# Performance work log

Measured on AMD Instinct MI355X. Metric: run time of the kernel, lower is better.

## Reference

```python
import jax, jax.numpy as jnp
import numpy as np

B, T, E, H = 8, 2048, 1024, 64

def setup_inputs() -> dict:
    key = jax.random.key(0)
    k1, k2, k3, k4 = jax.random.split(key, 4)
    x = jax.random.normal(k1, (B, T, E), dtype=jnp.float32)
    # Linear(E, H, bias=False) weights stored as [E, H] (x @ W)
    s = 1.0 / np.sqrt(E)
    Wk = jax.random.normal(k2, (E, H), dtype=jnp.float32) * s
    Wq = jax.random.normal(k3, (E, H), dtype=jnp.float32) * s
    Wv = jax.random.normal(k4, (E, H), dtype=jnp.float32) * s
    return {"x": x, "Wk": Wk, "Wq": Wq, "Wv": Wv}

def reference(x, Wk, Wq, Wv):
    _, t, e = x.shape
    k = jnp.einsum('bte,eh->bth', x, Wk)
    q = jnp.einsum('bte,eh->bth', x, Wq)
    v = jnp.einsum('bte,eh->bth', x, Wv)
    # NOTE: original scales by E**-0.5 (embedding dim), not head_size**-0.5
    wei = jnp.einsum('bqh,bkh->bqk', q, k) * (e ** -0.5)
    causal = jnp.tril(jnp.ones((t, t), dtype=bool))
    wei = jnp.where(causal, wei, -jnp.inf)
    wei = jax.nn.softmax(wei, axis=-1)
    out = jnp.einsum('bqk,bkh->bqh', wei, v)
    return out
```

## Files before the change

### kernel.cpp

```cpp
#include <hip/hip_runtime.h>

typedef unsigned short u16;
typedef unsigned int u32;
typedef __bf16 bf16x8 __attribute__((ext_vector_type(8)));
typedef __bf16 bf16x4 __attribute__((ext_vector_type(4)));
typedef float f32x4 __attribute__((ext_vector_type(4)));

constexpr int Bn = 8, Tn = 2048, En = 1024, Hn = 64;
constexpr int Mrows = Bn * Tn;
constexpr float CEXP = 0.03125f * 1.4426950408889634f;

__device__ __forceinline__ u16 f2bf(float f) {
  u32 u = __float_as_uint(f);
  return (u16)((u + 0x7fffu + ((u >> 16) & 1u)) >> 16);
}

__device__ __forceinline__ void gload16(const void* g, void* l) {
  __builtin_amdgcn_global_load_lds(
      (const __attribute__((address_space(1))) void*)g,
      (__attribute__((address_space(3))) void*)l, 16, 0, 0);
}

__global__ __launch_bounds__(256) void wt_kernel(
    const float* __restrict__ Wk, const float* __restrict__ Wq,
    const float* __restrict__ Wv, u16* __restrict__ Wt) {
  __shared__ u16 tile[64][72];
  const int mat = blockIdx.x >> 4;
  const int k0 = (blockIdx.x & 15) * 64;
  const float* W = (mat == 0) ? Wk : (mat == 1) ? Wq : Wv;
  const int t = threadIdx.x;
  {
    const int kl = t >> 2;
    const int h0 = (t & 3) * 16;
    const float4* src = (const float4*)(W + (size_t)(k0 + kl) * Hn + h0);
#pragma unroll
    for (int i = 0; i < 4; ++i) {
      float4 v = src[i];
      tile[h0 + 4 * i + 0][kl] = f2bf(v.x);
      tile[h0 + 4 * i + 1][kl] = f2bf(v.y);
      tile[h0 + 4 * i + 2][kl] = f2bf(v.z);
      tile[h0 + 4 * i + 3][kl] = f2bf(v.w);
    }
  }
  __syncthreads();
  {
    const int hl = t >> 2;
    const int kk = (t & 3) * 16;
    uint4 a = *(const uint4*)&tile[hl][kk];
    uint4 b = *(const uint4*)&tile[hl][kk + 8];
    u16* dst = Wt + (size_t)mat * Hn * En + (size_t)hl * En + k0 + kk;
    *(uint4*)dst = a;
    *(uint4*)(dst + 8) = b;
  }
}

__global__ __launch_bounds__(256, 2) void qkv_kernel(
    const float* __restrict__ x, const u16* __restrict__ Wt,
    u16* __restrict__ Kb16, u16* __restrict__ Qb16, u16* __restrict__ Vt16) {
  constexpr int BK = 64;
  __shared__ __align__(16) float xs[3][32 * BK];
  const int t = threadIdx.x;
  const int w = t >> 6, lane = t & 63;
  const int quad = lane >> 4, l16 = lane & 15;
  const int r0 = blockIdx.x * 32;

  const int rj0 = w * 8 + (lane >> 4);
  const int rj1 = rj0 + 4;
  const float* gsrc0 = x + (size_t)(r0 + rj0) * En + (((lane & 15) ^ (rj0 & 15)) << 2);
  const float* gsrc1 = x + (size_t)(r0 + rj1) * En + (((lane & 15) ^ (rj1 & 15)) << 2);

  const u16* wpb = Wt + (size_t)l16 * En + quad * 8;

  int ofs[2][2];
#pragma unroll
  for (int ks = 0; ks < 2; ++ks) {
    ofs[ks][0] = ((ks * 8 + quad * 2) ^ l16) << 2;
    ofs[ks][1] = ((ks * 8 + quad * 2 + 1) ^ l16) << 2;
  }

  f32x4 acc[3][2];
#pragma unroll
  for (int i = 0; i < 3; ++i)
#pragma unroll
    for (int nt = 0; nt < 2; ++nt) acc[i][nt] = (f32x4){0.f, 0.f, 0.f, 0.f};

  bf16x8 afA[3][2], afB[3][2];

#define STAGE(P, K0)                              \
  do {                                            \
    gload16(gsrc0 + (K0), (P) + w * 512);         \
    gload16(gsrc1 + (K0), (P) + w * 512 + 256);   \
  } while (0)

#define LOADA(DST, K0)                                                              \
  do {                                                                              \
    _Pragma("unroll") for (int i_ = 0; i_ < 3; ++i_)                                \
        _Pragma("unroll") for (int ks_ = 0; ks_ < 2; ++ks_)                         \
            DST[i_][ks_] = *(const bf16x8*)(wpb + (size_t)((3 * w + i_) * 16) * En + \
                                            (K0) + ks_ * 32);                       \
  } while (0)

#define CVT8(LO, HI, R)                                       \
  do {                                                        \
    R[0] = (__bf16)LO[0]; R[1] = (__bf16)LO[1];               \
    R[2] = (__bf16)LO[2]; R[3] = (__bf16)LO[3];               \
    R[4] = (__bf16)HI[0]; R[5] = (__bf16)HI[1];               \
    R[6] = (__bf16)HI[2]; R[7] = (__bf16)HI[3];               \
  } while (0)

#define COMPUTE(P, AF)                                                             \
  do {                                                                             \
    const float* xa_ = (P) + l16 * 64;                                             \
    const float* xb_ = (P) + (l16 + 16) * 64;                                      \
    _Pragma("unroll") for (int ks_ = 0; ks_ < 2; ++ks_) {                          \
      f32x4 lo0_ = *(const f32x4*)(xa_ + ofs[ks_][0]);                             \
      f32x4 hi0_ = *(const f32x4*)(xa_ + ofs[ks_][1]);                             \
      f32x4 lo1_ = *(const f32x4*)(xb_ + ofs[ks_][0]);                             \
      f32x4 hi1_ = *(const f32x4*)(xb_ + ofs[ks_][1]);                             \
      bf16x8 b0_, b1_;                                                             \
      CVT8(lo0_, hi0_, b0_);                                                       \
      CVT8(lo1_, hi1_, b1_);                                                       \
      _Pragma("unroll") for (int i_ = 0; i_ < 3; ++i_) {                           \
        acc[i_][0] = __builtin_amdgcn_mfma_f32_16x16x32_bf16(AF[i_][ks_], b0_,     \
                                                             acc[i_][0], 0, 0, 0); \
        acc[i_][1] = __builtin_amdgcn_mfma_f32_16x16x32_bf16(AF[i_][ks_], b1_,     \
                                                             acc[i_][1], 0, 0, 0); \
      }                                                                            \
    }                                                                              \
  } while (0)

#define WAITBAR(N)                                          \
  do {                                                      \
    asm volatile("s_waitcnt vmcnt(" #N ")" ::: "memory");   \
    __builtin_amdgcn_s_barrier();                           \
    asm volatile("" ::: "memory");                          \
  } while (0)

  float* p0 = &xs[0][0];
  float* p1 = &xs[1][0];
  float* p2 = &xs[2][0];

  STAGE(p0, 0);
  STAGE(p1, BK);
  LOADA(afA, 0);

  for (int tt = 0; tt < 16; tt += 2) {
    WAITBAR(8);
    LOADA(afB, (tt + 1) * 64);
    asm volatile("" ::: "memory");
    if (tt + 2 < 16) STAGE(p2, (tt + 2) * 64);
    COMPUTE(p0, afA);

    if (tt == 14) {
      WAITBAR(6);
    } else {
      WAITBAR(8);
    }
    if (tt + 2 < 16) LOADA(afA, (tt + 2) * 64);
    asm volatile("" ::: "memory");
    if (tt + 3 < 16) STAGE(p0, (tt + 3) * 64);
    COMPUTE(p1, afB);

    float* tmp = p0; p0 = p2; p2 = p1; p1 = tmp;
  }

#undef STAGE
#undef LOADA
#undef CVT8
#undef COMPUTE
#undef WAITBAR

#pragma unroll
  for (int i = 0; i < 3; ++i) {
    const int mt = 3 * w + i;
    const int mat = mt >> 2, ht = mt & 3;
#pragma unroll
    for (int nt = 0; nt < 2; ++nt) {
      const int row = r0 + nt * 16 + l16;
      f32x4 a = acc[i][nt];
      if (mat < 2) {
        u16* dst = ((mat == 0) ? Kb16 : Qb16) + (size_t)row * Hn + ht * 16 + quad * 4;
        uint2 pk;
        pk.x = (u32)f2bf(a[0]) | ((u32)f2bf(a[1]) << 16);
        pk.y = (u32)f2bf(a[2]) | ((u32)f2bf(a[3]) << 16);
        *(uint2*)dst = pk;
      } else {
        const int bb = row >> 11, tt = row & 2047;
        u16* base = Vt16 + ((size_t)bb * 64) * Tn + tt;
#pragma unroll
        for (int r = 0; r < 4; ++r)
          base[(size_t)(ht * 16 + quad * 4 + r) * Tn] = f2bf(a[r]);
      }
    }
  }
}

__global__ __launch_bounds__(256, 2) void attn_kernel(
    const u16* __restrict__ Qb16, const u16* __restrict__ Kb16,
    const u16* __restrict__ Vt16, float* __restrict__ out) {
  __shared__ u16 pt[2][4][2][16][40];
  __shared__ float l_sh[2][4][16];
  __shared__ float o_sh[2][4][16][68];

  const int idx = blockIdx.x;
  const int b = idx & 7;
  const int tq = 63 - (idx >> 3);
  const int w = threadIdx.x >> 6, lane = threadIdx.x & 63;
  const int quad = lane >> 4, l16 = lane & 15;
  const int qbase = tq * 32;
  const int limit = qbase + 32;
  const int ch = ((limit + 127) >> 7) << 5;
  const int lo = w * ch;
  const int hi = min(lo + ch, limit);
  const int qa_abs = qbase + l16;
  const int qb_abs = qbase + 16 + l16;

  const u16* Kp = Kb16 + (size_t)b * Tn * Hn;
  const u16* Vp = Vt16 + (size_t)b * 64 * Tn;

  const u16* qrowA = Qb16 + ((size_t)b * Tn + qa_abs) * Hn + quad * 8;
  const u16* qrowB = qrowA + (size_t)16 * Hn;
  const bf16x8 qa0 = *(const bf16x8*)(qrowA);
  const bf16x8 qa1 = *(const bf16x8*)(qrowA + 32);
  const bf16x8 qb0 = *(const bf16x8*)(qrowB);
  const bf16x8 qb1 = *(const bf16x8*)(qrowB + 32);

  f32x4 oA0 = {0.f, 0.f, 0.f, 0.f}, oA1 = oA0, oA2 = oA0, oA3 = oA0;
  f32x4 oB0 = oA0, oB1 = oA0, oB2 = oA0, oB3 = oA0;
  f32x4 laccA = oA0, laccB = oA0;

#pragma unroll 2
  for (int kb = lo; kb < hi; kb += 32) {
    const int par = (kb >> 5) & 1;
    const u16* krow0 = Kp + (size_t)(kb + l16) * Hn + quad * 8;
    const u16* krow1 = krow0 + (size_t)16 * Hn;
    const bf16x8 k0lo = *(const bf16x8*)(krow0);
    const bf16x8 k0hi = *(const bf16x8*)(krow0 + 32);
    const bf16x8 k1lo = *(const bf16x8*)(krow1);
    const bf16x8 k1hi = *(const bf16x8*)(krow1 + 32);

    const f32x4 z = {0.f, 0.f, 0.f, 0.f};
    f32x4 s0a = __builtin_amdgcn_mfma_f32_16x16x32_bf16(k0lo, qa0, z, 0, 0, 0);
    s0a = __builtin_amdgcn_mfma_f32_16x16x32_bf16(k0hi, qa1, s0a, 0, 0, 0);
    f32x4 s1a = __builtin_amdgcn_mfma_f32_16x16x32_bf16(k1lo, qa0, z, 0, 0, 0);
    s1a = __builtin_amdgcn_mfma_f32_16x16x32_bf16(k1hi, qa1, s1a, 0, 0, 0);
    f32x4 s0b = __builtin_amdgcn_mfma_f32_16x16x32_bf16(k0lo, qb0, z, 0, 0, 0);
    s0b = __builtin_amdgcn_mfma_f32_16x16x32_bf16(k0hi, qb1, s0b, 0, 0, 0);
    f32x4 s1b = __builtin_amdgcn_mfma_f32_16x16x32_bf16(k1lo, qb0, z, 0, 0, 0);
    s1b = __builtin_amdgcn_mfma_f32_16x16x32_bf16(k1hi, qb1, s1b, 0, 0, 0);

    if (kb + 15 > qbase) {
#pragma unroll
      for (int r = 0; r < 4; ++r)
        if (kb + quad * 4 + r > qa_abs) s0a[r] = -3.0e38f;
    }
    if (kb + 31 > qbase) {
#pragma unroll
      for (int r = 0; r < 4; ++r)
        if (kb + 16 + quad * 4 + r > qa_abs) s1a[r] = -3.0e38f;
    }
    if (kb + 15 > qbase + 16) {
#pragma unroll
      for (int r = 0; r < 4; ++r)
        if (kb + quad * 4 + r > qb_abs) s0b[r] = -3.0e38f;
    }
    if (kb + 31 > qbase + 16) {
#pragma unroll
      for (int r = 0; r < 4; ++r)
        if (kb + 16 + quad * 4 + r > qb_abs) s1b[r] = -3.0e38f;
    }

    f32x4 pa0, pa1, pb0v, pb1v;
#pragma unroll
    for (int r = 0; r < 4; ++r) {
      pa0[r] = __builtin_amdgcn_exp2f(s0a[r] * CEXP);
      pa1[r] = __builtin_amdgcn_exp2f(s1a[r] * CEXP);
      pb0v[r] = __builtin_amdgcn_exp2f(s0b[r] * CEXP);
      pb1v[r] = __builtin_amdgcn_exp2f(s1b[r] * CEXP);
    }
    laccA += pa0;
    laccA += pa1;
    laccB += pb0v;
    laccB += pb1v;

    {
      bf16x4 wa0, wa1, wb0, wb1;
      wa0[0] = (__bf16)pa0[0]; wa0[1] = (__bf16)pa0[1];
      wa0[2] = (__bf16)pa0[2]; wa0[3] = (__bf16)pa0[3];
      wa1[0] = (__bf16)pa1[0]; wa1[1] = (__bf16)pa1[1];
      wa1[2] = (__bf16)pa1[2]; wa1[3] = (__bf16)pa1[3];
      wb0[0] = (__bf16)pb0v[0]; wb0[1] = (__bf16)pb0v[1];
      wb0[2] = (__bf16)pb0v[2]; wb0[3] = (__bf16)pb0v[3];
      wb1[0] = (__bf16)pb1v[0]; wb1[1] = (__bf16)pb1v[1];
      wb1[2] = (__bf16)pb1v[2]; wb1[3] = (__bf16)pb1v[3];
      *(bf16x4*)&pt[par][w][0][l16][quad * 4] = wa0;
      *(bf16x4*)&pt[par][w][0][l16][16 + quad * 4] = wa1;
      *(bf16x4*)&pt[par][w][1][l16][quad * 4] = wb0;
      *(bf16x4*)&pt[par][w][1][l16][16 + quad * 4] = wb1;
    }
    const bf16x8 pba = *(const bf16x8*)&pt[par][w][0][l16][quad * 8];
    const bf16x8 pbb = *(const bf16x8*)&pt[par][w][1][l16][quad * 8];

    const u16* vrow = Vp + (size_t)l16 * Tn + kb + quad * 8;
    const bf16x8 v0 = *(const bf16x8*)(vrow);
    const bf16x8 v1 = *(const bf16x8*)(vrow + (size_t)16 * Tn);
    const bf16x8 v2 = *(const bf16x8*)(vrow + (size_t)32 * Tn);
    const bf16x8 v3 = *(const bf16x8*)(vrow + (size_t)48 * Tn);

    oA0 = __builtin_amdgcn_mfma_f32_16x16x32_bf16(v0, pba, oA0, 0, 0, 0);
    oA1 = __builtin_amdgcn_mfma_f32_16x16x32_bf16(v1, pba, oA1, 0, 0, 0);
    oA2 = __builtin_amdgcn_mfma_f32_16x16x32_bf16(v2, pba, oA2, 0, 0, 0);
    oA3 = __builtin_amdgcn_mfma_f32_16x16x32_bf16(v3, pba, oA3, 0, 0, 0);
    oB0 = __builtin_amdgcn_mfma_f32_16x16x32_bf16(v0, pbb, oB0, 0, 0, 0);
    oB1 = __builtin_amdgcn_mfma_f32_16x16x32_bf16(v1, pbb, oB1, 0, 0, 0);
    oB2 = __builtin_amdgcn_mfma_f32_16x16x32_bf16(v2, pbb, oB2, 0, 0, 0);
    oB3 = __builtin_amdgcn_mfma_f32_16x16x32_bf16(v3, pbb, oB3, 0, 0, 0);
  }

  float la = (laccA[0] + laccA[1]) + (laccA[2] + laccA[3]);
  la += __shfl_xor(la, 16);
  la += __shfl_xor(la, 32);
  float lb = (laccB[0] + laccB[1]) + (laccB[2] + laccB[3]);
  lb += __shfl_xor(lb, 16);
  lb += __shfl_xor(lb, 32);
  if (quad == 0) {
    l_sh[0][w][l16] = la;
    l_sh[1][w][l16] = lb;
  }
  *(f32x4*)&o_sh[0][w][l16][0 * 16 + quad * 4] = oA0;
  *(f32x4*)&o_sh[0][w][l16][1 * 16 + quad * 4] = oA1;
  *(f32x4*)&o_sh[0][w][l16][2 * 16 + quad * 4] = oA2;
  *(f32x4*)&o_sh[0][w][l16][3 * 16 + quad * 4] = oA3;
  *(f32x4*)&o_sh[1][w][l16][0 * 16 + quad * 4] = oB0;
  *(f32x4*)&o_sh[1][w][l16][1 * 16 + quad * 4] = oB1;
  *(f32x4*)&o_sh[1][w][l16][2 * 16 + quad * 4] = oB2;
  *(f32x4*)&o_sh[1][w][l16][3 * 16 + quad * 4] = oB3;
  __syncthreads();

  const int qq = threadIdx.x >> 4, dq = threadIdx.x & 15;
#pragma unroll
  for (int tl = 0; tl < 2; ++tl) {
    float lg = 0.f;
    f32x4 acc = {0.f, 0.f, 0.f, 0.f};
#pragma unroll
    for (int ww = 0; ww < 4; ++ww) {
      lg += l_sh[tl][ww][qq];
      acc += *(const f32x4*)&o_sh[tl][ww][qq][dq * 4];
    }
    acc *= (1.f / lg);
    *(f32x4*)(out + ((size_t)b * Tn + qbase + tl * 16 + qq) * Hn + dq * 4) = acc;
  }
}

extern "C" void kernel_launch(void* const* d_in, const int* in_sizes, int n_in,
                              void* d_out, int out_size, void* d_ws, size_t ws_size,
                              hipStream_t stream) {
  const void* x = nullptr;
  const void* Ws[3] = {nullptr, nullptr, nullptr};
  int wj = 0;
  for (int i = 0; i < n_in; ++i) {
    if (in_sizes[i] == Bn * Tn * En) x = d_in[i];
    else if (wj < 3) Ws[wj++] = d_in[i];
  }
  const float* Wk = (const float*)Ws[0];
  const float* Wq = (const float*)Ws[1];
  const float* Wv = (const float*)Ws[2];

  u16* Kb16 = (u16*)d_ws;
  u16* Qb16 = Kb16 + (size_t)Mrows * Hn;
  u16* Vt16 = Qb16 + (size_t)Mrows * Hn;
  u16* Wt   = Vt16 + (size_t)Mrows * Hn;

  wt_kernel<<<48, 256, 0, stream>>>(Wk, Wq, Wv, Wt);
  qkv_kernel<<<Mrows / 32, 256, 0, stream>>>((const float*)x, Wt, Kb16, Qb16, Vt16);
  attn_kernel<<<Bn * (Tn / 32), 256, 0, stream>>>(Qb16, Kb16, Vt16, (float*)d_out);
}
```

Baseline: 142.8 us.

## Restructure QKV projection so each wave owns 16 rows and all outputs

New measurement: 165.5 us. +15.9%, slower.

```diff
diff --git a/kernel.cpp b/kernel.cpp
--- a/kernel.cpp
+++ b/kernel.cpp
@@ -54,50 +54,59 @@
   }
 }
 
-__global__ __launch_bounds__(256, 2) void qkv_kernel(
+__global__ __launch_bounds__(128, 1) void qkv_kernel(
     const float* __restrict__ x, const u16* __restrict__ Wt,
     u16* __restrict__ Kb16, u16* __restrict__ Qb16, u16* __restrict__ Vt16) {
-  constexpr int BK = 64;
-  __shared__ __align__(16) float xs[3][32 * BK];
+  __shared__ __align__(16) float xs[2][3][1024];
   const int t = threadIdx.x;
   const int w = t >> 6, lane = t & 63;
   const int quad = lane >> 4, l16 = lane & 15;
-  const int r0 = blockIdx.x * 32;
-
-  const int rj0 = w * 8 + (lane >> 4);
-  const int rj1 = rj0 + 4;
-  const float* gsrc0 = x + (size_t)(r0 + rj0) * En + (((lane & 15) ^ (rj0 & 15)) << 2);
-  const float* gsrc1 = x + (size_t)(r0 + rj1) * En + (((lane & 15) ^ (rj1 & 15)) << 2);
+  const int r0w = blockIdx.x * 32 + w * 16;
+
+  const float* gs0;
+  const float* gs1;
+  const float* gs2;
+  const float* gs3;
+  {
+    const int rr0 = 0 * 4 + (lane >> 4);
+    const int rr1 = 1 * 4 + (lane >> 4);
+    const int rr2 = 2 * 4 + (lane >> 4);
+    const int rr3 = 3 * 4 + (lane >> 4);
+    gs0 = x + (size_t)(r0w + rr0) * En + (((lane & 15) ^ (rr0 & 15)) << 2);
+    gs1 = x + (size_t)(r0w + rr1) * En + (((lane & 15) ^ (rr1 & 15)) << 2);
+    gs2 = x + (size_t)(r0w + rr2) * En + (((lane & 15) ^ (rr2 & 15)) << 2);
+    gs3 = x + (size_t)(r0w + rr3) * En + (((lane & 15) ^ (rr3 & 15)) << 2);
+  }
 
   const u16* wpb = Wt + (size_t)l16 * En + quad * 8;
 
   int ofs[2][2];
 #pragma unroll
   for (int ks = 0; ks < 2; ++ks) {
-    ofs[ks][0] = ((ks * 8 + quad * 2) ^ l16) << 2;
-    ofs[ks][1] = ((ks * 8 + quad * 2 + 1) ^ l16) << 2;
-  }
-
-  f32x4 acc[3][2];
-#pragma unroll
-  for (int i = 0; i < 3; ++i)
-#pragma unroll
-    for (int nt = 0; nt < 2; ++nt) acc[i][nt] = (f32x4){0.f, 0.f, 0.f, 0.f};
-
-  bf16x8 afA[3][2], afB[3][2];
-
-#define STAGE(P, K0)                              \
-  do {                                            \
-    gload16(gsrc0 + (K0), (P) + w * 512);         \
-    gload16(gsrc1 + (K0), (P) + w * 512 + 256);   \
-  } while (0)
-
-#define LOADA(DST, K0)                                                              \
-  do {                                                                              \
-    _Pragma("unroll") for (int i_ = 0; i_ < 3; ++i_)                                \
-        _Pragma("unroll") for (int ks_ = 0; ks_ < 2; ++ks_)                         \
-            DST[i_][ks_] = *(const bf16x8*)(wpb + (size_t)((3 * w + i_) * 16) * En + \
-                                            (K0) + ks_ * 32);                       \
+    ofs[ks][0] = (((ks * 8 + quad * 2 + 0) ^ l16) << 2);
+    ofs[ks][1] = (((ks * 8 + quad * 2 + 1) ^ l16) << 2);
+  }
+
+  f32x4 acc[12];
+#pragma unroll
+  for (int i = 0; i < 12; ++i) acc[i] = (f32x4){0.f, 0.f, 0.f, 0.f};
+
+  bf16x8 SA[2][12], C[12];
+
+#define STAGE(T)                                                      \
+  do {                                                                \
+    char* lb_ = (char*)&xs[w][(T) % 3][0];                            \
+    gload16(gs0 + (T) * 64, lb_ + 0 * 1024);                          \
+    gload16(gs1 + (T) * 64, lb_ + 1 * 1024);                          \
+    gload16(gs2 + (T) * 64, lb_ + 2 * 1024);                          \
+    gload16(gs3 + (T) * 64, lb_ + 3 * 1024);                          \
+  } while (0)
+
+#define LOADA(DST, T, KS)                                                       \
+  do {                                                                          \
+    _Pragma("unroll") for (int m_ = 0; m_ < 12; ++m_)                           \
+        DST[m_] = *(const bf16x8*)(wpb + (size_t)(m_ * 16) * En + (T) * 64 +    \
+                                   (KS) * 32);                                  \
   } while (0)
 
 #define CVT8(LO, HI, R)                                       \
@@ -108,89 +117,66 @@
     R[6] = (__bf16)HI[2]; R[7] = (__bf16)HI[3];               \
   } while (0)
 
-#define COMPUTE(P, AF)                                                             \
-  do {                                                                             \
-    const float* xa_ = (P) + l16 * 64;                                             \
-    const float* xb_ = (P) + (l16 + 16) * 64;                                      \
-    _Pragma("unroll") for (int ks_ = 0; ks_ < 2; ++ks_) {                          \
-      f32x4 lo0_ = *(const f32x4*)(xa_ + ofs[ks_][0]);                             \
-      f32x4 hi0_ = *(const f32x4*)(xa_ + ofs[ks_][1]);                             \
-      f32x4 lo1_ = *(const f32x4*)(xb_ + ofs[ks_][0]);                             \
-      f32x4 hi1_ = *(const f32x4*)(xb_ + ofs[ks_][1]);                             \
-      bf16x8 b0_, b1_;                                                             \
-      CVT8(lo0_, hi0_, b0_);                                                       \
-      CVT8(lo1_, hi1_, b1_);                                                       \
-      _Pragma("unroll") for (int i_ = 0; i_ < 3; ++i_) {                           \
-        acc[i_][0] = __builtin_amdgcn_mfma_f32_16x16x32_bf16(AF[i_][ks_], b0_,     \
-                                                             acc[i_][0], 0, 0, 0); \
-        acc[i_][1] = __builtin_amdgcn_mfma_f32_16x16x32_bf16(AF[i_][ks_], b1_,     \
-                                                             acc[i_][1], 0, 0, 0); \
-      }                                                                            \
-    }                                                                              \
-  } while (0)
-
-#define WAITBAR(N)                                          \
+#define COMPUTE_KS(T, KS, AF)                                                  \
+  do {                                                                         \
+    const float* xa_ = &xs[w][(T) % 3][l16 * 64];                              \
+    f32x4 lo_ = *(const f32x4*)(xa_ + ofs[KS][0]);                             \
+    f32x4 hi_ = *(const f32x4*)(xa_ + ofs[KS][1]);                             \
+    bf16x8 b_;                                                                 \
+    CVT8(lo_, hi_, b_);                                                        \
+    _Pragma("unroll") for (int m_ = 0; m_ < 12; ++m_)                          \
+        acc[m_] = __builtin_amdgcn_mfma_f32_16x16x32_bf16(AF[m_], b_,          \
+                                                          acc[m_], 0, 0, 0);   \
+  } while (0)
+
+#define WAITV(N)                                            \
   do {                                                      \
     asm volatile("s_waitcnt vmcnt(" #N ")" ::: "memory");   \
-    __builtin_amdgcn_s_barrier();                           \
-    asm volatile("" ::: "memory");                          \
-  } while (0)
-
-  float* p0 = &xs[0][0];
-  float* p1 = &xs[1][0];
-  float* p2 = &xs[2][0];
-
-  STAGE(p0, 0);
-  STAGE(p1, BK);
-  LOADA(afA, 0);
-
-  for (int tt = 0; tt < 16; tt += 2) {
-    WAITBAR(8);
-    LOADA(afB, (tt + 1) * 64);
-    asm volatile("" ::: "memory");
-    if (tt + 2 < 16) STAGE(p2, (tt + 2) * 64);
-    COMPUTE(p0, afA);
-
-    if (tt == 14) {
-      WAITBAR(6);
+  } while (0)
+
+  STAGE(0);
+  STAGE(1);
+  LOADA(SA[0], 0, 0);
+
+#pragma unroll
+  for (int tt = 0; tt < 16; ++tt) {
+    LOADA(C, tt, 1);
+    if (tt + 1 < 16) LOADA(SA[(tt + 1) & 1], tt + 1, 0);
+    if (tt + 2 < 16) STAGE(tt + 2);
+    if (tt <= 13) {
+      WAITV(44);
+    } else if (tt == 14) {
+      WAITV(40);
     } else {
-      WAITBAR(8);
-    }
-    if (tt + 2 < 16) LOADA(afA, (tt + 2) * 64);
-    asm volatile("" ::: "memory");
-    if (tt + 3 < 16) STAGE(p0, (tt + 3) * 64);
-    COMPUTE(p1, afB);
-
-    float* tmp = p0; p0 = p2; p2 = p1; p1 = tmp;
+      WAITV(24);
+    }
+    COMPUTE_KS(tt, 0, SA[tt & 1]);
+    COMPUTE_KS(tt, 1, C);
   }
 
 #undef STAGE
 #undef LOADA
 #undef CVT8
-#undef COMPUTE
-#undef WAITBAR
-
-#pragma unroll
-  for (int i = 0; i < 3; ++i) {
-    const int mt = 3 * w + i;
+#undef COMPUTE_KS
+#undef WAITV
+
+  const int row = r0w + l16;
+#pragma unroll
+  for (int mt = 0; mt < 12; ++mt) {
     const int mat = mt >> 2, ht = mt & 3;
-#pragma unroll
-    for (int nt = 0; nt < 2; ++nt) {
-      const int row = r0 + nt * 16 + l16;
-      f32x4 a = acc[i][nt];
-      if (mat < 2) {
-        u16* dst = ((mat == 0) ? Kb16 : Qb16) + (size_t)row * Hn + ht * 16 + quad * 4;
-        uint2 pk;
-        pk.x = (u32)f2bf(a[0]) | ((u32)f2bf(a[1]) << 16);
-        pk.y = (u32)f2bf(a[2]) | ((u32)f2bf(a[3]) << 16);
-        *(uint2*)dst = pk;
-      } else {
-        const int bb = row >> 11, tt = row & 2047;
-        u16* base = Vt16 + ((size_t)bb * 64) * Tn + tt;
-#pragma unroll
-        for (int r = 0; r < 4; ++r)
-          base[(size_t)(ht * 16 + quad * 4 + r) * Tn] = f2bf(a[r]);
-      }
+    f32x4 a = acc[mt];
+    if (mat < 2) {
+      u16* dst = ((mat == 0) ? Kb16 : Qb16) + (size_t)row * Hn + ht * 16 + quad * 4;
+      uint2 pk;
+      pk.x = (u32)f2bf(a[0]) | ((u32)f2bf(a[1]) << 16);
+      pk.y = (u32)f2bf(a[2]) | ((u32)f2bf(a[3]) << 16);
+      *(uint2*)dst = pk;
+    } else {
+      const int bb = row >> 11, ttr = row & 2047;
+      u16* base = Vt16 + ((size_t)bb * 64) * Tn + ttr;
+#pragma unroll
+      for (int r = 0; r < 4; ++r)
+        base[(size_t)(ht * 16 + quad * 4 + r) * Tn] = f2bf(a[r]);
     }
   }
 }
@@ -372,6 +358,6 @@
   u16* Wt   = Vt16 + (size_t)Mrows * Hn;
 
   wt_kernel<<<48, 256, 0, stream>>>(Wk, Wq, Wv, Wt);
-  qkv_kernel<<<Mrows / 32, 256, 0, stream>>>((const float*)x, Wt, Kb16, Qb16, Vt16);
+  qkv_kernel<<<Mrows / 32, 128, 0, stream>>>((const float*)x, Wt, Kb16, Qb16, Vt16);
   attn_kernel<<<Bn * (Tn / 32), 256, 0, stream>>>(Qb16, Kb16, Vt16, (float*)d_out);
 }
```
